# Optimization experiments

Hardware: AMD Instinct MI355X
Metric: run time of the kernel (lower is better)

Reference implementation:

```python
import jax, jax.numpy as jnp
import numpy as np

EMBED = 512
HEADS = 64
DK = EMBED // HEADS  # == n_wires_attn == 8
NW_FFN = 8
FFN = 2048
EPS = 1e-5


def _layernorm(x, g, b):
    mu = jnp.mean(x, axis=-1, keepdims=True)
    var = jnp.var(x, axis=-1, keepdims=True)
    return (x - mu) * jax.lax.rsqrt(var + EPS) * g + b


def setup_inputs() -> dict:
    key = jax.random.key(0)
    ks = jax.random.split(key, 12)
    d = {
        "x": jax.random.normal(ks[0], (4, 1024, EMBED), dtype=jnp.float32),
        # attention quantum RX params (one per wire, shared across heads/tokens)
        "phi": jax.random.normal(ks[1], (DK,), dtype=jnp.float32) * 0.1,
        # combine_heads linear
        "Wc": jax.random.normal(ks[2], (EMBED, EMBED), dtype=jnp.float32) / np.sqrt(EMBED),
        "bc": jnp.zeros((EMBED,), dtype=jnp.float32),
        # FFN quantum RY params
        "theta": jax.random.normal(ks[3], (NW_FFN,), dtype=jnp.float32) * 0.1,
        "W1": jax.random.normal(ks[4], (NW_FFN, FFN), dtype=jnp.float32) / np.sqrt(NW_FFN),
        "b1": jnp.zeros((FFN,), dtype=jnp.float32),
        "W2": jax.random.normal(ks[5], (FFN, EMBED), dtype=jnp.float32) / np.sqrt(FFN),
        "b2": jnp.zeros((EMBED,), dtype=jnp.float32),
        "g1": jnp.ones((EMBED,), dtype=jnp.float32),
        "be1": jnp.zeros((EMBED,), dtype=jnp.float32),
        "g2": jnp.ones((EMBED,), dtype=jnp.float32),
        "be2": jnp.zeros((EMBED,), dtype=jnp.float32),
    }
    return d


def reference(x, phi, Wc, bc, theta, W1, b1, W2, b2, g1, be1, g2, be2):
    B, S, E = x.shape
    # --- quantum attention projections ---
    # Per head-row of DK features: RX(x_i) encoder then trainable RX(phi_i),
    xh = x.reshape(B, S, HEADS, DK)
    qkv = jnp.cos(xh + phi)                     # [B,S,H,DK]
    qkv = jnp.transpose(qkv, (0, 2, 1, 3))      # [B,H,S,DK]
    scores = jnp.einsum('bhqd,bhkd->bhqk', qkv, qkv) / jnp.sqrt(jnp.float32(DK))
    attn = jax.nn.softmax(scores, axis=-1)
    out = jnp.einsum('bhqk,bhkd->bhqd', attn, qkv)
    out = jnp.transpose(out, (0, 2, 1, 3)).reshape(B, S, E)
    attn_out = out @ Wc.T if False else out @ Wc + bc  # combine_heads linear
    x1 = _layernorm(x + attn_out, g1, be1)
    # --- quantum FFN: RX(x_i) then trainable RY(theta_i) -> <Z> = cos(x_i)*cos(theta_i)
    qout = jnp.cos(x1[..., :NW_FFN]) * jnp.cos(theta)   # [B,S,NW_FFN]
    h = jax.nn.relu(qout @ W1 + b1)
    ffn_out = h @ W2 + b2
    return _layernorm(x1 + ffn_out, g2, be2)
```

## Files before the change

### kernel.cpp

```cpp
#include <hip/hip_runtime.h>
#include <hip/hip_bf16.h>
#include <math.h>

#define B 4
#define S 1024
#define E 512
#define H 64
#define DK 8
#define FFN 2048
#define BS (B*S)

#define CSCALE 0.7141879f

#if __has_builtin(__builtin_amdgcn_exp2f)
#define EXP2F(x) __builtin_amdgcn_exp2f(x)
#else
#define EXP2F(x) exp2f(x)
#endif

typedef __attribute__((ext_vector_type(8))) short short8;
typedef __attribute__((ext_vector_type(4))) float float4a;

union U8 { short8 v; unsigned u[4]; };
union F4 { float4a v; float f[4]; };

__device__ __forceinline__ unsigned short f2bf(float f) {
    unsigned u = __builtin_bit_cast(unsigned, f);
    u = (u + 0x7fffu + ((u >> 16) & 1u)) >> 16;
    return (unsigned short)u;
}
__device__ __forceinline__ float bf2f(unsigned short h) {
    return __builtin_bit_cast(float, (unsigned)h << 16);
}
__device__ __forceinline__ unsigned packbf(float a, float b) {
    return __builtin_amdgcn_perm(__builtin_bit_cast(unsigned, a),
                                 __builtin_bit_cast(unsigned, b), 0x07060302u);
}
__device__ __forceinline__ unsigned packbf_rn(float a, float b) {
    return ((unsigned)f2bf(a) << 16) | f2bf(b);
}
__device__ __forceinline__ int pidx(int k) {
    return (k & ~31) | (((k >> 2) & 3) << 3) | (((k >> 4) & 1) << 2) | (k & 3);
}

__global__ __launch_bounds__(512) void attn_conv_kernel(const float* __restrict__ x,
                                                        const float* __restrict__ phi,
                                                        const float* __restrict__ Wc,
                                                        const float* __restrict__ W2,
                                                        const float* __restrict__ W1,
                                                        const float* __restrict__ b1,
                                                        unsigned short* __restrict__ Afrag,
                                                        unsigned short* __restrict__ W2f,
                                                        unsigned short* __restrict__ Wcf,
                                                        unsigned short* __restrict__ W1f) {
    __shared__ unsigned short kv[(S + 16) * DK];
    __shared__ unsigned short vtp[9][S + 8];
    int bid = blockIdx.x;
    int tid = threadIdx.x;

    if (bid >= 1024) {
        int idx = (bid - 1024) * 512 + tid;
        if (idx < 131072) {
            int lane = idx & 63, c = idx >> 6;
            int ntile = c >> 6, kb32 = c & 63;
            int g = lane >> 4, col = lane & 15;
            int n = ntile * 16 + col, kb = kb32 * 32;
            short8 o;
            #pragma unroll
            for (int j = 0; j < 8; j++) {
                int k = kb + 16 * (j >> 2) + 4 * g + (j & 3);
                o[j] = (short)f2bf(W2[(size_t)k * 512 + n]);
            }
            *(short8*)&W2f[(size_t)idx * 8] = o;
        } else if (idx < 163840) {
            int i2 = idx - 131072;
            int lane = i2 & 63, c = i2 >> 6;
            int ntile = c >> 4, kb32 = c & 15;
            int g = lane >> 4, col = lane & 15;
            int n = ntile * 16 + col, kb = kb32 * 32;
            short8 o;
            #pragma unroll
            for (int j = 0; j < 8; j++)
                o[j] = (short)f2bf(Wc[(size_t)(kb + g * 8 + j) * 512 + n]);
            *(short8*)&Wcf[(size_t)i2 * 8] = o;
        } else {
            int i3 = idx - 163840;
            int lane = i3 & 63, c = i3 >> 6;
            int g = lane >> 4, col = lane & 15;
            int f = (c >> 1) * 32 + (c & 1) * 16 + col;
            short8 o = {0,0,0,0,0,0,0,0};
            if (g == 0) {
                #pragma unroll
                for (int j = 0; j < 8; j++) o[j] = (short)f2bf(W1[j * FFN + f]);
            } else if (g == 1) {
                o[0] = (short)f2bf(b1[f]);
            }
            *(short8*)&W1f[(size_t)i3 * 8] = o;
        }
        return;
    }

    int head = bid >> 2, qquad = bid & 3;
    int b = head >> 6, hh = head & 63;

    float ph[DK];
    #pragma unroll
    for (int d = 0; d < DK; d++) ph[d] = phi[d];

    const short8 z8 = {0,0,0,0,0,0,0,0};
    {
        int r2 = tid * 2;
        unsigned short vb[8][2];
        #pragma unroll
        for (int j = 0; j < 2; j++) {
            const float* xp = x + ((size_t)(b * S + r2 + j)) * E + hh * DK;
            float4 u = *(const float4*)xp;
            float4 v = *(const float4*)(xp + 4);
            float c[8] = {__cosf(u.x+ph[0]), __cosf(u.y+ph[1]), __cosf(u.z+ph[2]), __cosf(u.w+ph[3]),
                          __cosf(v.x+ph[4]), __cosf(v.y+ph[5]), __cosf(v.z+ph[6]), __cosf(v.w+ph[7])};
            U8 kr;
            kr.u[0] = packbf_rn(c[1] * CSCALE, c[0] * CSCALE);
            kr.u[1] = packbf_rn(c[3] * CSCALE, c[2] * CSCALE);
            kr.u[2] = packbf_rn(c[5] * CSCALE, c[4] * CSCALE);
            kr.u[3] = packbf_rn(c[7] * CSCALE, c[6] * CSCALE);
            *(short8*)&kv[(r2 + j) * DK] = kr.v;
            #pragma unroll
            for (int d = 0; d < 8; d++) vb[d][j] = f2bf(c[d]);
        }
        int pr = pidx(r2);
        #pragma unroll
        for (int d = 0; d < 8; d++)
            *(unsigned*)&vtp[d][pr] = (unsigned)vb[d][0] | ((unsigned)vb[d][1] << 16);
        *(unsigned*)&vtp[8][pr] = 0x3F803F80u;
    }
    if (tid < 16) *(short8*)&kv[(S + tid) * DK] = z8;
    __syncthreads();

    int w = tid >> 6, lane = tid & 63, col = lane & 15, g = lane >> 4;
    bool g0 = (g == 0);
    int q0 = qquad * 256 + w * 32;
    const float4a zc = {0.f,0.f,0.f,0.f};

    short8 aq[2];
    #pragma unroll
    for (int t = 0; t < 2; t++)
        aq[t] = g0 ? *(const short8*)&kv[(q0 + t*16 + col) * DK] : z8;

    float4a acc[2];
    acc[0] = zc; acc[1] = zc;

    int vrow = col < 8 ? col : 8;
    const unsigned short* vbase = &vtp[vrow][0];

    int off0 = g0 ? col * DK : S * DK;
    int off1 = g0 ? (16 + col) * DK : S * DK;
    int stepo = g0 ? 32 * DK : 0;

    for (int kb = 0; kb < S; kb += 32) {
        short8 bk0 = *(const short8*)&kv[off0];
        short8 bk1 = *(const short8*)&kv[off1];
        off0 += stepo; off1 += stepo;
        short8 vf = *(const short8*)(vbase + kb + g * 8);
        #pragma unroll
        for (int t = 0; t < 2; t++) {
            float4a s0 = __builtin_amdgcn_mfma_f32_16x16x32_bf16(bk0, aq[t], zc, 0,0,0);
            float4a s1 = __builtin_amdgcn_mfma_f32_16x16x32_bf16(bk1, aq[t], zc, 0,0,0);
            F4 S0, S1; S0.v = s0; S1.v = s1;
            float e00 = EXP2F(S0.f[0]);
            float e01 = EXP2F(S0.f[1]);
            float e02 = EXP2F(S0.f[2]);
            float e03 = EXP2F(S0.f[3]);
            float e10 = EXP2F(S1.f[0]);
            float e11 = EXP2F(S1.f[1]);
            float e12 = EXP2F(S1.f[2]);
            float e13 = EXP2F(S1.f[3]);
            U8 pf;
            pf.u[0] = packbf(e01, e00);
            pf.u[1] = packbf(e03, e02);
            pf.u[2] = packbf(e11, e10);
            pf.u[3] = packbf(e13, e12);
            acc[t] = __builtin_amdgcn_mfma_f32_16x16x32_bf16(vf, pf.v, acc[t], 0,0,0);
        }
    }
    int lp8 = ((hh & 3) * 16 + col) * 8;
    #pragma unroll
    for (int t = 0; t < 2; t++) {
        F4 a; a.v = acc[t];
        float denom = __shfl(a.f[0], 32 + col);
        float inv = __builtin_amdgcn_rcpf(denom);
        if (g < 2) {
            int chunk = (hh >> 2) * 256 + (b * 64 + qquad * 16 + w * 2 + t);
            uint2 o;
            o.x = packbf_rn(a.f[1] * inv, a.f[0] * inv);
            o.y = packbf_rn(a.f[3] * inv, a.f[2] * inv);
            *(uint2*)&Afrag[(size_t)chunk * 512 + lp8 + g * 4] = o;
        }
    }
}

__global__ __launch_bounds__(512) void combine_ln1(const unsigned short* __restrict__ Afrag,
                                                   const unsigned short* __restrict__ Wcf,
                                                   const float* __restrict__ bc,
                                                   const float* __restrict__ x,
                                                   const float* __restrict__ g1,
                                                   const float* __restrict__ be1,
                                                   float* __restrict__ x1out,
                                                   unsigned short* __restrict__ qoutbf,
                                                   const float* __restrict__ theta) {
    __shared__ unsigned short As[16 * 64 * 8];
    __shared__ float xout[16][516];
    int tt = blockIdx.x;
    int tid = threadIdx.x;

    for (int i = tid; i < 1024; i += 512)
        *(short8*)&As[i * 8] =
            *(const short8*)&Afrag[((size_t)((i >> 6) * 256 + tt) * 64 + (i & 63)) * 8];
    __syncthreads();

    int w = tid >> 6, lane = tid & 63, col = lane & 15, g = lane >> 4;
    const float4a zc = {0.f,0.f,0.f,0.f};
    float4a acc[4];
    #pragma unroll
    for (int nt = 0; nt < 4; nt++) acc[nt] = zc;

    for (int kb32 = 0; kb32 < 16; kb32++) {
        short8 af = *(const short8*)&As[(kb32 * 64 + lane) * 8];
        #pragma unroll
        for (int nt = 0; nt < 4; nt++) {
            short8 bf = *(const short8*)&Wcf[((size_t)((w * 4 + nt) * 16 + kb32) * 64 + lane) * 8];
            acc[nt] = __builtin_amdgcn_mfma_f32_16x16x32_bf16(af, bf, acc[nt], 0, 0, 0);
        }
    }
    #pragma unroll
    for (int nt = 0; nt < 4; nt++) {
        int n = w * 64 + nt * 16 + col;
        float bb = bc[n];
        #pragma unroll
        for (int r = 0; r < 4; r++)
            xout[g * 4 + r][n] = acc[nt][r] + bb;
    }
    __syncthreads();

    int hl = lane >> 5, l = lane & 31;
    int token = w * 2 + hl;
    int e0 = l * 16;
    size_t grow = ((size_t)tt * 16 + token) * 512;
    float v[16];
    float s = 0.f, sq = 0.f;
    #pragma unroll
    for (int u = 0; u < 4; u++) {
        float4 xv = *(const float4*)&x[grow + e0 + u * 4];
        float4 pv = *(const float4*)&xout[token][e0 + u * 4];
        float a0 = xv.x + pv.x, a1 = xv.y + pv.y, a2 = xv.z + pv.z, a3 = xv.w + pv.w;
        v[u*4] = a0; v[u*4+1] = a1; v[u*4+2] = a2; v[u*4+3] = a3;
        s += a0 + a1 + a2 + a3;
        sq += a0*a0 + a1*a1 + a2*a2 + a3*a3;
    }
    #pragma unroll
    for (int off = 1; off <= 16; off <<= 1) {
        s  += __shfl_xor(s, off);
        sq += __shfl_xor(sq, off);
    }
    float mu = s * (1.f / 512.f);
    float var = sq * (1.f / 512.f) - mu * mu;
    float rstd = rsqrtf(var + 1e-5f);
    float y[16];
    #pragma unroll
    for (int u = 0; u < 4; u++) {
        float4 gv = *(const float4*)&g1[e0 + u * 4];
        float4 bv = *(const float4*)&be1[e0 + u * 4];
        y[u*4]   = (v[u*4]   - mu) * rstd * gv.x + bv.x;
        y[u*4+1] = (v[u*4+1] - mu) * rstd * gv.y + bv.y;
        y[u*4+2] = (v[u*4+2] - mu) * rstd * gv.z + bv.z;
        y[u*4+3] = (v[u*4+3] - mu) * rstd * gv.w + bv.w;
        float4 o = make_float4(y[u*4], y[u*4+1], y[u*4+2], y[u*4+3]);
        *(float4*)&x1out[grow + e0 + u * 4] = o;
    }
    if (l == 0) {
        U8 q;
        q.u[0] = packbf_rn(__cosf(y[1]) * __cosf(theta[1]), __cosf(y[0]) * __cosf(theta[0]));
        q.u[1] = packbf_rn(__cosf(y[3]) * __cosf(theta[3]), __cosf(y[2]) * __cosf(theta[2]));
        q.u[2] = packbf_rn(__cosf(y[5]) * __cosf(theta[5]), __cosf(y[4]) * __cosf(theta[4]));
        q.u[3] = packbf_rn(__cosf(y[7]) * __cosf(theta[7]), __cosf(y[6]) * __cosf(theta[6]));
        *(short8*)&qoutbf[((size_t)tt * 16 + token) * 8] = q.v;
    }
}

__global__ __launch_bounds__(512) void ffn_mfma(const unsigned short* __restrict__ qbf,
                                                const unsigned short* __restrict__ W1fg,
                                                const unsigned short* __restrict__ W2f,
                                                const float* __restrict__ b2,
                                                unsigned short* __restrict__ Cbf) {
    __shared__ unsigned short w1x[FFN * 16];
    int tid = threadIdx.x;
    #pragma unroll
    for (int i = 0; i < 8; i++) {
        int d = tid + i * 512;
        int f = d >> 1, gg = d & 1;
        int kb32 = f >> 5, half = (f >> 4) & 1, fc = f & 15;
        int src = ((kb32 * 2 + half) * 64 + gg * 16 + fc);
        *(short8*)&w1x[f * 16 + gg * 8] = *(const short8*)&W1fg[(size_t)src * 8];
    }
    __syncthreads();

    int w = tid >> 6, lane = tid & 63, col = lane & 15, g = lane >> 4;
    int mw = blockIdx.x * 256 + w * 32;
    int ntile0 = blockIdx.y * 2;
    const short8 z8 = {0,0,0,0,0,0,0,0};
    const short8 one8 = {(short)0x3F80,0,0,0,0,0,0,0};
    const float4a zc = {0.f,0.f,0.f,0.f};

    short8 qf[2];
    #pragma unroll
    for (int t = 0; t < 2; t++)
        qf[t] = (g == 0) ? *(const short8*)&qbf[(size_t)(mw + t * 16 + col) * 8]
                         : (g == 1 ? one8 : z8);

    float4a acc[2][2];
    acc[0][0] = zc; acc[0][1] = zc; acc[1][0] = zc; acc[1][1] = zc;

    const unsigned short* w2p0 = W2f + (size_t)(ntile0 * 64) * 512 + lane * 8;
    const unsigned short* w2p1 = W2f + (size_t)((ntile0 + 1) * 64) * 512 + lane * 8;

    for (int kb32 = 0; kb32 < 64; kb32++) {
        int kb = kb32 * 32;
        short8 w1f0 = (g < 2) ? *(const short8*)&w1x[(kb + col) * 16 + g * 8] : z8;
        short8 w1f1 = (g < 2) ? *(const short8*)&w1x[(kb + 16 + col) * 16 + g * 8] : z8;
        short8 af0 = *(const short8*)(w2p0 + (size_t)kb32 * 512);
        short8 af1 = *(const short8*)(w2p1 + (size_t)kb32 * 512);
        #pragma unroll
        for (int t = 0; t < 2; t++) {
            float4a h0 = __builtin_amdgcn_mfma_f32_16x16x32_bf16(w1f0, qf[t], zc, 0,0,0);
            float4a h1 = __builtin_amdgcn_mfma_f32_16x16x32_bf16(w1f1, qf[t], zc, 0,0,0);
            F4 H0, H1; H0.v = h0; H1.v = h1;
            float e00 = fmaxf(H0.f[0], 0.f);
            float e01 = fmaxf(H0.f[1], 0.f);
            float e02 = fmaxf(H0.f[2], 0.f);
            float e03 = fmaxf(H0.f[3], 0.f);
            float e10 = fmaxf(H1.f[0], 0.f);
            float e11 = fmaxf(H1.f[1], 0.f);
            float e12 = fmaxf(H1.f[2], 0.f);
            float e13 = fmaxf(H1.f[3], 0.f);
            U8 pf;
            pf.u[0] = packbf(e01, e00);
            pf.u[1] = packbf(e03, e02);
            pf.u[2] = packbf(e11, e10);
            pf.u[3] = packbf(e13, e12);
            acc[t][0] = __builtin_amdgcn_mfma_f32_16x16x32_bf16(af0, pf.v, acc[t][0], 0,0,0);
            acc[t][1] = __builtin_amdgcn_mfma_f32_16x16x32_bf16(af1, pf.v, acc[t][1], 0,0,0);
        }
    }
    int n0 = ntile0 * 16;
    #pragma unroll
    for (int nt = 0; nt < 2; nt++) {
        float4 bb = *(const float4*)&b2[n0 + nt * 16 + 4 * g];
        #pragma unroll
        for (int t = 0; t < 2; t++) {
            F4 a; a.v = acc[t][nt];
            uint2 o;
            o.x = packbf_rn(a.f[1] + bb.y, a.f[0] + bb.x);
            o.y = packbf_rn(a.f[3] + bb.w, a.f[2] + bb.z);
            *(uint2*)&Cbf[(size_t)(mw + t * 16 + col) * 512 + n0 + nt * 16 + 4 * g] = o;
        }
    }
}

__global__ __launch_bounds__(256) void ln_kernel(const float* a,
                                                 const unsigned short* __restrict__ r,
                                                 const float* __restrict__ g,
                                                 const float* __restrict__ be,
                                                 float* out) {
    int t = blockIdx.x, tid = threadIdx.x;
    size_t base = (size_t)t * E;
    int e0 = tid * 2;
    float2 av = *(const float2*)&a[base + e0];
    unsigned rv = *(const unsigned*)&r[base + e0];
    float v0 = av.x + bf2f((unsigned short)(rv & 0xffff));
    float v1 = av.y + bf2f((unsigned short)(rv >> 16));
    float s  = v0 + v1;
    float sq = v0 * v0 + v1 * v1;
    #pragma unroll
    for (int off = 32; off > 0; off >>= 1) {
        s  += __shfl_down(s, off);
        sq += __shfl_down(sq, off);
    }
    __shared__ float ls[4], lq[4];
    int wave = tid >> 6, lane = tid & 63;
    if (lane == 0) { ls[wave] = s; lq[wave] = sq; }
    __syncthreads();
    if (tid == 0) {
        float SS = ls[0] + ls[1] + ls[2] + ls[3];
        float QQ = lq[0] + lq[1] + lq[2] + lq[3];
        float mu = SS * (1.f / E);
        float var = QQ * (1.f / E) - mu * mu;
        ls[0] = mu;
        lq[0] = rsqrtf(var + 1e-5f);
    }
    __syncthreads();
    float mu = ls[0], rstd = lq[0];
    float2 gv = *(const float2*)&g[e0];
    float2 bv = *(const float2*)&be[e0];
    float y0 = (v0 - mu) * rstd * gv.x + bv.x;
    float y1 = (v1 - mu) * rstd * gv.y + bv.y;
    *(float2*)&out[base + e0] = make_float2(y0, y1);
}

extern "C" void kernel_launch(void* const* d_in, const int* in_sizes, int n_in,
                              void* d_out, int out_size, void* d_ws, size_t ws_size,
                              hipStream_t stream) {
    const float* x     = (const float*)d_in[0];
    const float* phi   = (const float*)d_in[1];
    const float* Wc    = (const float*)d_in[2];
    const float* bc    = (const float*)d_in[3];
    const float* theta = (const float*)d_in[4];
    const float* W1    = (const float*)d_in[5];
    const float* b1    = (const float*)d_in[6];
    const float* W2    = (const float*)d_in[7];
    const float* b2    = (const float*)d_in[8];
    const float* g1    = (const float*)d_in[9];
    const float* be1   = (const float*)d_in[10];
    const float* g2    = (const float*)d_in[11];
    const float* be2   = (const float*)d_in[12];
    float* out = (float*)d_out;

    float* ws = (float*)d_ws;
    unsigned short* Afrag  = (unsigned short*)ws;
    unsigned short* W2f    = (unsigned short*)(ws + 1048576);
    unsigned short* Wcf    = (unsigned short*)(ws + 1572864);
    unsigned short* W1f    = (unsigned short*)(ws + 1703936);
    unsigned short* qoutbf = (unsigned short*)(ws + 1736704);

    attn_conv_kernel<<<1360, 512, 0, stream>>>(x, phi, Wc, W2, W1, b1,
                                               Afrag, W2f, Wcf, W1f);
    combine_ln1<<<256, 512, 0, stream>>>(Afrag, Wcf, bc, x, g1, be1,
                                         out, qoutbf, theta);
    ffn_mfma<<<dim3(16, 16), 512, 0, stream>>>(qoutbf, W1f, W2f, b2, Afrag);
    ln_kernel<<<BS, 256, 0, stream>>>(out, Afrag, g2, be2, out);
}
```

Before: 161.3 us.

## Fuse final layernorm into FFN kernel via last-block atomic counters

Removes the separate ln_kernel launch by fusing the second residual+layernorm into the FFN kernel. Each FFN block increments per-row-tile atomic counters after writing its output tile, and the block that completes a 16-token tile (the 16th contributor across blockIdx.y) does the layernorm for those tokens. Counters are zeroed in combine_ln1. This saves a launch and a re-read pass but adds fences, atomics and serialized tail work on the last-arriving blocks.

```diff
diff --git a/kernel.cpp b/kernel.cpp
--- a/kernel.cpp
+++ b/kernel.cpp
@@ -206,11 +206,13 @@
                                                    const float* __restrict__ be1,
                                                    float* __restrict__ x1out,
                                                    unsigned short* __restrict__ qoutbf,
-                                                   const float* __restrict__ theta) {
+                                                   const float* __restrict__ theta,
+                                                   int* __restrict__ ctr) {
     __shared__ unsigned short As[16 * 64 * 8];
     __shared__ float xout[16][516];
     int tt = blockIdx.x;
     int tid = threadIdx.x;
+    if (tid == 0) ctr[tt] = 0;
 
     for (int i = tid; i < 1024; i += 512)
         *(short8*)&As[i * 8] =
@@ -286,12 +288,17 @@
     }
 }
 
-__global__ __launch_bounds__(512) void ffn_mfma(const unsigned short* __restrict__ qbf,
-                                                const unsigned short* __restrict__ W1fg,
-                                                const unsigned short* __restrict__ W2f,
-                                                const float* __restrict__ b2,
-                                                unsigned short* __restrict__ Cbf) {
+__global__ __launch_bounds__(512) void ffn_ln2(const unsigned short* __restrict__ qbf,
+                                               const unsigned short* __restrict__ W1fg,
+                                               const unsigned short* __restrict__ W2f,
+                                               const float* __restrict__ b2,
+                                               const float* __restrict__ g2,
+                                               const float* __restrict__ be2,
+                                               unsigned short* __restrict__ Cbf,
+                                               float* out,
+                                               int* __restrict__ ctr) {
     __shared__ unsigned short w1x[FFN * 16];
+    __shared__ int flags[16];
     int tid = threadIdx.x;
     #pragma unroll
     for (int i = 0; i < 8; i++) {
@@ -363,46 +370,55 @@
             *(uint2*)&Cbf[(size_t)(mw + t * 16 + col) * 512 + n0 + nt * 16 + 4 * g] = o;
         }
     }
-}
-
-__global__ __launch_bounds__(256) void ln_kernel(const float* a,
-                                                 const unsigned short* __restrict__ r,
-                                                 const float* __restrict__ g,
-                                                 const float* __restrict__ be,
-                                                 float* out) {
-    int t = blockIdx.x, tid = threadIdx.x;
-    size_t base = (size_t)t * E;
-    int e0 = tid * 2;
-    float2 av = *(const float2*)&a[base + e0];
-    unsigned rv = *(const unsigned*)&r[base + e0];
-    float v0 = av.x + bf2f((unsigned short)(rv & 0xffff));
-    float v1 = av.y + bf2f((unsigned short)(rv >> 16));
-    float s  = v0 + v1;
-    float sq = v0 * v0 + v1 * v1;
-    #pragma unroll
-    for (int off = 32; off > 0; off >>= 1) {
-        s  += __shfl_down(s, off);
-        sq += __shfl_down(sq, off);
-    }
-    __shared__ float ls[4], lq[4];
-    int wave = tid >> 6, lane = tid & 63;
-    if (lane == 0) { ls[wave] = s; lq[wave] = sq; }
-    __syncthreads();
-    if (tid == 0) {
-        float SS = ls[0] + ls[1] + ls[2] + ls[3];
-        float QQ = lq[0] + lq[1] + lq[2] + lq[3];
-        float mu = SS * (1.f / E);
-        float var = QQ * (1.f / E) - mu * mu;
-        ls[0] = mu;
-        lq[0] = rsqrtf(var + 1e-5f);
-    }
-    __syncthreads();
-    float mu = ls[0], rstd = lq[0];
-    float2 gv = *(const float2*)&g[e0];
-    float2 bv = *(const float2*)&be[e0];
-    float y0 = (v0 - mu) * rstd * gv.x + bv.x;
-    float y1 = (v1 - mu) * rstd * gv.y + bv.y;
-    *(float2*)&out[base + e0] = make_float2(y0, y1);
+
+    __threadfence();
+    __syncthreads();
+    if (tid < 16)
+        flags[tid] = (atomicAdd(&ctr[blockIdx.x * 16 + tid], 1) == 15) ? 1 : 0;
+    __syncthreads();
+
+    int hl = lane >> 5, l = lane & 31;
+    int e0 = l * 16;
+    for (int tl = 0; tl < 16; tl++) {
+        if (flags[tl] == 0) continue;
+        __threadfence();
+        int token = (blockIdx.x * 16 + tl) * 16 + w * 2 + hl;
+        size_t grow = (size_t)token * 512;
+        const uint4* fp = (const uint4*)&Cbf[grow + e0];
+        uint4 f0v = fp[0], f1v = fp[1];
+        unsigned fu[8] = {f0v.x, f0v.y, f0v.z, f0v.w, f1v.x, f1v.y, f1v.z, f1v.w};
+        float v[16];
+        float s = 0.f, sq = 0.f;
+        #pragma unroll
+        for (int u = 0; u < 4; u++) {
+            float4 xv = *(const float4*)&out[grow + e0 + u * 4];
+            float a0 = xv.x + bf2f((unsigned short)(fu[u*2] & 0xffff));
+            float a1 = xv.y + bf2f((unsigned short)(fu[u*2] >> 16));
+            float a2 = xv.z + bf2f((unsigned short)(fu[u*2+1] & 0xffff));
+            float a3 = xv.w + bf2f((unsigned short)(fu[u*2+1] >> 16));
+            v[u*4] = a0; v[u*4+1] = a1; v[u*4+2] = a2; v[u*4+3] = a3;
+            s += a0 + a1 + a2 + a3;
+            sq += a0*a0 + a1*a1 + a2*a2 + a3*a3;
+        }
+        #pragma unroll
+        for (int off = 1; off <= 16; off <<= 1) {
+            s  += __shfl_xor(s, off);
+            sq += __shfl_xor(sq, off);
+        }
+        float mu = s * (1.f / 512.f);
+        float var = sq * (1.f / 512.f) - mu * mu;
+        float rstd = rsqrtf(var + 1e-5f);
+        #pragma unroll
+        for (int u = 0; u < 4; u++) {
+            float4 gv = *(const float4*)&g2[e0 + u * 4];
+            float4 bv = *(const float4*)&be2[e0 + u * 4];
+            float4 o = make_float4((v[u*4]   - mu) * rstd * gv.x + bv.x,
+                                   (v[u*4+1] - mu) * rstd * gv.y + bv.y,
+                                   (v[u*4+2] - mu) * rstd * gv.z + bv.z,
+                                   (v[u*4+3] - mu) * rstd * gv.w + bv.w);
+            *(float4*)&out[grow + e0 + u * 4] = o;
+        }
+    }
 }
 
 extern "C" void kernel_launch(void* const* d_in, const int* in_sizes, int n_in,
@@ -429,11 +445,12 @@
     unsigned short* Wcf    = (unsigned short*)(ws + 1572864);
     unsigned short* W1f    = (unsigned short*)(ws + 1703936);
     unsigned short* qoutbf = (unsigned short*)(ws + 1736704);
+    int*            ctr    = (int*)(ws + 1753088);
 
     attn_conv_kernel<<<1360, 512, 0, stream>>>(x, phi, Wc, W2, W1, b1,
                                                Afrag, W2f, Wcf, W1f);
     combine_ln1<<<256, 512, 0, stream>>>(Afrag, Wcf, bc, x, g1, be1,
-                                         out, qoutbf, theta);
-    ffn_mfma<<<dim3(16, 16), 512, 0, stream>>>(qoutbf, W1f, W2f, b2, Afrag);
-    ln_kernel<<<BS, 256, 0, stream>>>(out, Afrag, g2, be2, out);
-}
+                                         out, qoutbf, theta, ctr);
+    ffn_ln2<<<dim3(16, 16), 512, 0, stream>>>(qoutbf, W1f, W2f, b2, g2, be2,
+                                              Afrag, out, ctr);
+}
```

Result: slower. 322.6 us (+99.9%).
